# Kernel tuning notes

Hardware: AMD Instinct MI355X
Metric: run time of the kernel (lower is better)

## Reference

```python
import jax, jax.numpy as jnp
import numpy as np

B, T, D, H = 512, 256, 64, 256


def setup_inputs() -> dict:
    key = jax.random.key(0)
    ks = jax.random.split(key, 12)
    X = jax.random.normal(ks[0], (B, T, D), dtype=jnp.float32)
    M = (jax.random.uniform(ks[1], (B, T, D)) < 0.7).astype(jnp.float32)
    # time since last observation, hours
    Delta = jax.random.uniform(ks[2], (B, T, D), dtype=jnp.float32) * 5.0
    x_mean = jax.random.normal(ks[3], (D,), dtype=jnp.float32) * 0.1
    s = 1.0 / np.sqrt(D)
    sh = 1.0 / np.sqrt(H)
    # input-decay Linear(D->D), hidden-decay Linear(D->H)
    W_gx = jax.random.uniform(ks[4], (D, D), minval=-s, maxval=s, dtype=jnp.float32)
    b_gx = jnp.zeros((D,), jnp.float32)
    W_gh = jax.random.uniform(ks[5], (D, H), minval=-s, maxval=s, dtype=jnp.float32)
    b_gh = jnp.zeros((H,), jnp.float32)
    # stacked gate weights for [z, r, h_tilde]
    W_x = jax.random.uniform(ks[6], (3, D, H), minval=-s, maxval=s, dtype=jnp.float32)
    W_h = jax.random.uniform(ks[7], (3, H, H), minval=-sh, maxval=sh, dtype=jnp.float32)
    W_m = jax.random.uniform(ks[8], (3, D, H), minval=-s, maxval=s, dtype=jnp.float32)
    b_g = jnp.zeros((3, H), jnp.float32)
    W_cls = jax.random.uniform(ks[9], (H, 1), minval=-sh, maxval=sh, dtype=jnp.float32)
    b_cls = jnp.zeros((1,), jnp.float32)
    return dict(X=X, M=M, Delta=Delta, x_mean=x_mean,
                W_gx=W_gx, b_gx=b_gx, W_gh=W_gh, b_gh=b_gh,
                W_x=W_x, W_h=W_h, W_m=W_m, b_g=b_g,
                W_cls=W_cls, b_cls=b_cls)


def reference(X, M, Delta, x_mean, W_gx, b_gx, W_gh, b_gh,
              W_x, W_h, W_m, b_g, W_cls, b_cls):
    Bn, Tn, Dn = X.shape
    Hn = W_h.shape[-1]

    def step(carry, inp):
        h, x_prev = carry          # [B,H], [B,D]
        x, m, d = inp              # each [B,D]
        gamma_x = jnp.exp(-jax.nn.relu(d @ W_gx + b_gx))   # [B,D]
        gamma_h = jnp.exp(-jax.nn.relu(d @ W_gh + b_gh))   # [B,H]
        # mean imputation with input decay
        x_hat = m * x + (1.0 - m) * (gamma_x * x_prev + (1.0 - gamma_x) * x_mean)
        hd = gamma_h * h                                   # hidden decay
        z = jax.nn.sigmoid(x_hat @ W_x[0] + hd @ W_h[0] + m @ W_m[0] + b_g[0])
        r = jax.nn.sigmoid(x_hat @ W_x[1] + hd @ W_h[1] + m @ W_m[1] + b_g[1])
        h_tilde = jnp.tanh(x_hat @ W_x[2] + (r * hd) @ W_h[2] + m @ W_m[2] + b_g[2])
        h_new = (1.0 - z) * hd + z * h_tilde
        x_prev_new = m * x + (1.0 - m) * x_prev            # carry last observation
        return (h_new, x_prev_new), None

    h0 = jnp.zeros((Bn, Hn), X.dtype)
    xp0 = jnp.zeros((Bn, Dn), X.dtype)
    xs = (jnp.swapaxes(X, 0, 1), jnp.swapaxes(M, 0, 1), jnp.swapaxes(Delta, 0, 1))
    (h, _), _ = jax.lax.scan(step, (h0, xp0), xs)
    return (h @ W_cls + b_cls)[:, 0]   # [B], classifier(h).squeeze(-1)
```

## Files before the change

kernel.cpp:

```cpp
#include <hip/hip_runtime.h>


constexpr int Bn = 512, Tn = 256, Dn = 64, Hn = 256;
constexpr int BB = 16, NBLK = Bn / BB;
constexpr int TC = 128;

typedef __attribute__((ext_vector_type(8))) short bf8_t;
typedef __attribute__((ext_vector_type(4))) float f4_t;

constexpr size_t OFF_WH  = 0;
constexpr size_t OFF_WX  = 196608;
constexpr size_t OFF_WM  = 245760;
constexpr size_t OFF_WGH = 294912;
constexpr size_t OFF_WGX = 311296;
constexpr int    PACK_SLOTS = 39424;

constexpr size_t GX_OFF  = (size_t)1 << 20;
constexpr size_t GH_OFF  = GX_OFF + (size_t)Bn * Tn * Dn * 4;
constexpr size_t WS_NEED = GH_OFF + (size_t)Bn * Tn * Hn * 2;

constexpr size_t GH2_OFF = (size_t)1 << 20;
constexpr size_t GX2_OFF = GH2_OFF + (size_t)Bn * Tn * Hn * 2;
constexpr size_t P2_OFF  = GX2_OFF;
constexpr size_t P2_SZ   = (size_t)3 * Bn * TC * Hn * 2;
constexpr size_t XH2_OFF = P2_OFF + P2_SZ;
constexpr size_t HST_OFF = XH2_OFF + (size_t)Bn * Tn * Dn * 2;
constexpr size_t WS_NEED3 = HST_OFF + (size_t)Bn * Hn * 2;

__device__ __forceinline__ unsigned short f2bf(float x) {
    union { float f; unsigned int u; } v; v.f = x;
    unsigned int r = (v.u + 0x7fffu + ((v.u >> 16) & 1u)) >> 16;
    return (unsigned short)r;
}
__device__ __forceinline__ float bf2f(unsigned short u) {
    union { unsigned int i; float f; } v; v.i = ((unsigned int)u) << 16; return v.f;
}
__device__ __forceinline__ bf8_t LD8(const short* p) { return *(const bf8_t*)p; }
__device__ __forceinline__ f4_t MF(bf8_t a, bf8_t b, f4_t c) {
    return __builtin_amdgcn_mfma_f32_16x16x32_bf16(a, b, c, 0, 0, 0);
}
__device__ __forceinline__ f4_t MFp(bf8_t a, const short* bp, f4_t c) {
    return MF(a, LD8(bp), c);
}
__device__ __forceinline__ const short* BA(const short* p, int ntG, int KT, int kt, int lane) {
    return p + (((size_t)ntG * KT + kt) * 64 + lane) * 8;
}
__device__ __forceinline__ void lds_sync() {
    __builtin_amdgcn_sched_barrier(0);
    asm volatile("s_waitcnt lgkmcnt(0)" ::: "memory");
    __builtin_amdgcn_s_barrier();
    __builtin_amdgcn_sched_barrier(0);
}

__global__ __launch_bounds__(256) void pack_weights(
    const float* __restrict__ W_gx, const float* __restrict__ W_gh,
    const float* __restrict__ W_x,  const float* __restrict__ W_h,
    const float* __restrict__ W_m,  short* __restrict__ out)
{
    const int slot = blockIdx.x * 256 + threadIdx.x;
    if (slot >= PACK_SLOTS) return;

    const float* w; int ldn, l, kt, j, kbase;
    if (slot < 24576) {
        int g = slot >> 13, rem = slot & 8191;
        int ntG = rem >> 9, r2 = rem & 511;
        kt = r2 >> 6; l = r2 & 63;
        j = ntG * 16 + (l & 15);
        w = W_h + (size_t)g * Hn * Hn; ldn = Hn;
    } else if (slot < 30720) {
        int s = slot - 24576;
        int g = s >> 11, rem = s & 2047;
        int ntG = rem >> 7, r2 = rem & 127;
        kt = r2 >> 6; l = r2 & 63;
        j = ntG * 16 + (l & 15);
        w = W_x + (size_t)g * Dn * Hn; ldn = Hn;
    } else if (slot < 36864) {
        int s = slot - 30720;
        int g = s >> 11, rem = s & 2047;
        int ntG = rem >> 7, r2 = rem & 127;
        kt = r2 >> 6; l = r2 & 63;
        j = ntG * 16 + (l & 15);
        w = W_m + (size_t)g * Dn * Hn; ldn = Hn;
    } else if (slot < 38912) {
        int s = slot - 36864;
        int ntG = s >> 7, r2 = s & 127;
        kt = r2 >> 6; l = r2 & 63;
        j = ntG * 16 + (l & 15);
        w = W_gh; ldn = Hn;
    } else {
        int s = slot - 38912;
        int ntG = s >> 7, r2 = s & 127;
        kt = r2 >> 6; l = r2 & 63;
        j = ntG * 16 + (l & 15);
        w = W_gx; ldn = Dn;
    }
    kbase = kt * 32 + ((l >> 4) << 3);
    bf8_t v;
    #pragma unroll
    for (int i = 0; i < 8; ++i)
        v[i] = (short)f2bf(w[(size_t)(kbase + i) * ldn + j]);
    *(bf8_t*)&out[(size_t)slot * 8] = v;
}

__global__ __launch_bounds__(256) void grud_prepass(
    const float* __restrict__ Dl, const float* __restrict__ b_gx,
    const float* __restrict__ b_gh, const short* __restrict__ pk,
    float* __restrict__ gx, unsigned short* __restrict__ gh)
{
    __shared__ short sDf[2 * 64 * 8];
    const int tid = threadIdx.x, w = tid >> 6, lane = tid & 63;
    const int bt = blockIdx.x >> 8, t = blockIdx.x & 255;
    const int b0 = bt * 16;
    const int c15 = lane & 15, rowb = (lane >> 4) * 4;

    if (w < 2) {
        const int row = lane & 15, cb = w * 32 + ((lane >> 4) << 3);
        const float* p = Dl + ((size_t)(b0 + row) * Tn + t) * Dn + cb;
        float4 a = *(const float4*)p, b = *(const float4*)(p + 4);
        bf8_t v;
        v[0]=(short)f2bf(a.x); v[1]=(short)f2bf(a.y); v[2]=(short)f2bf(a.z); v[3]=(short)f2bf(a.w);
        v[4]=(short)f2bf(b.x); v[5]=(short)f2bf(b.y); v[6]=(short)f2bf(b.z); v[7]=(short)f2bf(b.w);
        *(bf8_t*)&sDf[(w * 64 + lane) * 8] = v;
    }
    __syncthreads();
    bf8_t df0 = *(const bf8_t*)&sDf[lane * 8];
    bf8_t df1 = *(const bf8_t*)&sDf[(64 + lane) * 8];

    #pragma unroll
    for (int i = 0; i < 4; ++i) {
        const int ntG = 4 * w + i;
        f4_t acc = {0.f, 0.f, 0.f, 0.f};
        acc = MFp(df0, BA(pk + OFF_WGH, ntG, 2, 0, lane), acc);
        acc = MFp(df1, BA(pk + OFF_WGH, ntG, 2, 1, lane), acc);
        const int col = ntG * 16 + c15;
        const float bb = b_gh[col];
        #pragma unroll
        for (int q = 0; q < 4; ++q) {
            const int r = rowb + q;
            gh[((size_t)(b0 + r) * Tn + t) * Hn + col] =
                f2bf(__expf(-fmaxf(acc[q] + bb, 0.f)));
        }
    }
    {
        f4_t acc = {0.f, 0.f, 0.f, 0.f};
        acc = MFp(df0, BA(pk + OFF_WGX, w, 2, 0, lane), acc);
        acc = MFp(df1, BA(pk + OFF_WGX, w, 2, 1, lane), acc);
        const int col = w * 16 + c15;
        const float bb = b_gx[col];
        #pragma unroll
        for (int q = 0; q < 4; ++q) {
            const int r = rowb + q;
            gx[((size_t)(b0 + r) * Tn + t) * Dn + col] =
                __expf(-fmaxf(acc[q] + bb, 0.f));
        }
    }
}

__global__ __launch_bounds__(256) void grud_xhat(
    const float* __restrict__ X, const float* __restrict__ M,
    const float* __restrict__ x_mean, const float* __restrict__ gx,
    unsigned short* __restrict__ XH)
{
    const int g = blockIdx.x * 256 + threadIdx.x;
    const int b = g >> 6, d = g & 63;
    const float xm = x_mean[d];
    float xp = 0.f;
    const size_t base = (size_t)b * Tn * Dn + d;
    for (int t = 0; t < Tn; ++t) {
        const size_t idx = base + (size_t)t * Dn;
        const float x = X[idx], m = M[idx], gv = gx[idx];
        const float xh = m * x + (1.f - m) * (gv * xp + (1.f - gv) * xm);
        xp = m * x + (1.f - m) * xp;
        XH[idx] = f2bf(xh);
    }
}

__global__ __launch_bounds__(256) void grud_pgemm_c(
    const float* __restrict__ M, const unsigned short* __restrict__ XH,
    const float* __restrict__ b_g, const short* __restrict__ pk,
    unsigned short* __restrict__ P, int t0)
{
    const int tid = threadIdx.x, w = tid >> 6, lane = tid & 63;
    const int c15 = lane & 15;
    const int bblk = blockIdx.x >> 7;
    const int tl = blockIdx.x & (TC - 1);
    const int b0 = bblk * 16, t = t0 + tl;

    const size_t abase = ((size_t)(b0 + (lane & 15)) * Tn + t) * Dn + ((lane >> 4) << 3);
    bf8_t xf[2], mf[2];
    #pragma unroll
    for (int kt = 0; kt < 2; ++kt) {
        uint4 xa = *(const uint4*)&XH[abase + kt * 32];
        union { uint4 u; bf8_t b; } cvt; cvt.u = xa;
        xf[kt] = cvt.b;
        float4 a = *(const float4*)&M[abase + kt * 32];
        float4 b = *(const float4*)&M[abase + kt * 32 + 4];
        bf8_t v;
        v[0]=(short)f2bf(a.x); v[1]=(short)f2bf(a.y); v[2]=(short)f2bf(a.z); v[3]=(short)f2bf(a.w);
        v[4]=(short)f2bf(b.x); v[5]=(short)f2bf(b.y); v[6]=(short)f2bf(b.z); v[7]=(short)f2bf(b.w);
        mf[kt] = v;
    }

    const size_t btl = (size_t)blockIdx.x;
    #pragma unroll
    for (int i = 0; i < 12; ++i) {
        const int p = w * 12 + i;
        const int gg = p >> 4, ntG = p & 15;
        f4_t acc = {0.f, 0.f, 0.f, 0.f};
        acc = MFp(xf[0], BA(pk + OFF_WX + (size_t)gg * 16384, ntG, 2, 0, lane), acc);
        acc = MFp(xf[1], BA(pk + OFF_WX + (size_t)gg * 16384, ntG, 2, 1, lane), acc);
        acc = MFp(mf[0], BA(pk + OFF_WM + (size_t)gg * 16384, ntG, 2, 0, lane), acc);
        acc = MFp(mf[1], BA(pk + OFF_WM + (size_t)gg * 16384, ntG, 2, 1, lane), acc);
        const float bb = b_g[gg * Hn + ntG * 16 + c15];
        ushort4 o;
        o.x = f2bf(acc[0] + bb); o.y = f2bf(acc[1] + bb);
        o.z = f2bf(acc[2] + bb); o.w = f2bf(acc[3] + bb);
        *(ushort4*)&P[((btl * 3 + gg) * 16 + ntG) * 256 + lane * 4] = o;
    }
}

__global__ __launch_bounds__(512, 2) void grud_rec16(
    const float* __restrict__ W_cls, const float* __restrict__ b_cls,
    const short* __restrict__ pk, const unsigned short* __restrict__ gh,
    const unsigned short* __restrict__ P, unsigned short* __restrict__ hst,
    float* __restrict__ out, int t0, int lastc)
{
    __shared__ short sWh1[16 * 8 * 64 * 8];
    __shared__ unsigned short sh_hb[16][264];
    __shared__ short sA_rhd[8 * 64 * 8];

    const int tid = threadIdx.x, w = tid >> 6, lane = tid & 63;
    const int c15 = lane & 15, rowb = (lane >> 4) * 4;
    const int b0 = blockIdx.x * BB;
    unsigned short* hs = hst + (size_t)blockIdx.x * 16 * Hn;

    bf8_t whz[2][8], whh[2][8];
    #pragma unroll
    for (int nt = 0; nt < 2; ++nt)
        #pragma unroll
        for (int kt = 0; kt < 8; ++kt) {
            whz[nt][kt] = LD8(BA(pk + OFF_WH,             2 * w + nt, 8, kt, lane));
            whh[nt][kt] = LD8(BA(pk + OFF_WH + 2 * 65536, 2 * w + nt, 8, kt, lane));
        }
    for (int c = tid; c < 8192; c += 512)
        *(uint4*)&sWh1[c * 8] = *(const uint4*)&pk[OFF_WH + 65536 + (size_t)c * 8];

    if (t0 == 0) {
        for (int i = tid; i < 16 * 264; i += 512) (&sh_hb[0][0])[i] = 0;
    } else {
        for (int i = tid; i < 16 * 256; i += 512) {
            const int r = i >> 8, c = i & 255;
            float hv = bf2f(hs[i]);
            float gv = bf2f(gh[((size_t)(b0 + r) * Tn + t0) * Hn + c]);
            sh_hb[r][c] = f2bf(gv * hv);
        }
    }

    unsigned short ghcd[2][4];
    {
        const int t1 = (t0 + 1 < Tn) ? (t0 + 1) : (Tn - 1);
        #pragma unroll
        for (int nt = 0; nt < 2; ++nt)
            #pragma unroll
            for (int q = 0; q < 4; ++q)
                ghcd[nt][q] = gh[((size_t)(b0 + rowb + q) * Tn + t1) * Hn + w * 32 + nt * 16 + c15];
    }
    ushort4 pz[2], pr[2], ph[2];
    {
        const size_t pbl = (size_t)blockIdx.x * TC;
        #pragma unroll
        for (int nt = 0; nt < 2; ++nt) {
            pz[nt] = *(const ushort4*)&P[((pbl * 3 + 0) * 16 + 2 * w + nt) * 256 + lane * 4];
            pr[nt] = *(const ushort4*)&P[((pbl * 3 + 1) * 16 + 2 * w + nt) * 256 + lane * 4];
            ph[nt] = *(const ushort4*)&P[((pbl * 3 + 2) * 16 + 2 * w + nt) * 256 + lane * 4];
        }
    }
    float hd_cd[2][4], zz[2][4];
    const f4_t z4 = {0.f, 0.f, 0.f, 0.f};
    __syncthreads();

    for (int tl = 0; tl < TC; ++tl) {
        const int last = (tl == TC - 1);
        const int tnl  = last ? (TC - 1) : (tl + 1);
        const int tg2  = (t0 + tl + 2 < Tn) ? (t0 + tl + 2) : (Tn - 1);

        unsigned short ghcd_n[2][4];
        #pragma unroll
        for (int nt = 0; nt < 2; ++nt)
            #pragma unroll
            for (int q = 0; q < 4; ++q)
                ghcd_n[nt][q] = gh[((size_t)(b0 + rowb + q) * Tn + tg2) * Hn + w * 32 + nt * 16 + c15];
        ushort4 pz_n[2], pr_n[2], ph_n[2];
        {
            const size_t pbl = (size_t)blockIdx.x * TC + tnl;
            #pragma unroll
            for (int nt = 0; nt < 2; ++nt) {
                pz_n[nt] = *(const ushort4*)&P[((pbl * 3 + 0) * 16 + 2 * w + nt) * 256 + lane * 4];
                pr_n[nt] = *(const ushort4*)&P[((pbl * 3 + 1) * 16 + 2 * w + nt) * 256 + lane * 4];
                ph_n[nt] = *(const ushort4*)&P[((pbl * 3 + 2) * 16 + 2 * w + nt) * 256 + lane * 4];
            }
        }
        #pragma unroll
        for (int nt = 0; nt < 2; ++nt)
            #pragma unroll
            for (int q = 0; q < 4; ++q)
                hd_cd[nt][q] = bf2f(sh_hb[rowb + q][w * 32 + nt * 16 + c15]);

        f4_t aZ[2] = {z4, z4}, aR[2] = {z4, z4};
        #pragma unroll
        for (int kt = 0; kt < 8; ++kt) {
            union { uint4 u; bf8_t b; } hf;
            hf.u = *(const uint4*)&sh_hb[lane & 15][kt * 32 + ((lane >> 4) << 3)];
            bf8_t wr0 = LD8(&sWh1[((2 * w + 0) * 8 + kt) * 512 + lane * 8]);
            bf8_t wr1 = LD8(&sWh1[((2 * w + 1) * 8 + kt) * 512 + lane * 8]);
            aZ[0] = MF(hf.b, whz[0][kt], aZ[0]);
            aZ[1] = MF(hf.b, whz[1][kt], aZ[1]);
            aR[0] = MF(hf.b, wr0, aR[0]);
            aR[1] = MF(hf.b, wr1, aR[1]);
        }
        #pragma unroll
        for (int nt = 0; nt < 2; ++nt) {
            const int col = w * 32 + nt * 16 + c15;
            #pragma unroll
            for (int q = 0; q < 4; ++q) {
                const int r = rowb + q;
                float z  = 1.f / (1.f + __expf(-(aZ[nt][q] + bf2f(((const unsigned short*)&pz[nt])[q]))));
                float rr = 1.f / (1.f + __expf(-(aR[nt][q] + bf2f(((const unsigned short*)&pr[nt])[q]))));
                zz[nt][q] = z;
                sA_rhd[(w * 64 + ((col & 31) >> 3) * 16 + r) * 8 + (col & 7)] =
                    (short)f2bf(rr * hd_cd[nt][q]);
            }
        }
        lds_sync();

        f4_t aH[2] = {z4, z4};
        #pragma unroll
        for (int kt = 0; kt < 8; ++kt) {
            bf8_t rf = LD8(&sA_rhd[(kt * 64 + lane) * 8]);
            aH[0] = MF(rf, whh[0][kt], aH[0]);
            aH[1] = MF(rf, whh[1][kt], aH[1]);
        }
        #pragma unroll
        for (int nt = 0; nt < 2; ++nt) {
            const int col = w * 32 + nt * 16 + c15;
            #pragma unroll
            for (int q = 0; q < 4; ++q) {
                const int r = rowb + q;
                float pre = aH[nt][q] + bf2f(((const unsigned short*)&ph[nt])[q]);
                float a = fabsf(pre), e = __expf(-2.f * a);
                float th = copysignf((1.f - e) / (1.f + e), pre);
                float hn = (1.f - zz[nt][q]) * hd_cd[nt][q] + zz[nt][q] * th;
                float sv = last ? hn : hn * bf2f(ghcd[nt][q]);
                sh_hb[r][col] = f2bf(sv);
            }
        }
        lds_sync();

        #pragma unroll
        for (int nt = 0; nt < 2; ++nt) {
            #pragma unroll
            for (int q = 0; q < 4; ++q) ghcd[nt][q] = ghcd_n[nt][q];
            pz[nt] = pz_n[nt]; pr[nt] = pr_n[nt]; ph[nt] = ph_n[nt];
        }
    }

    if (!lastc) {
        for (int i = tid; i < 16 * 256; i += 512)
            hs[i] = sh_hb[i >> 8][i & 255];
    } else {
        #pragma unroll
        for (int rr2 = 0; rr2 < 2; ++rr2) {
            const int row = w * 2 + rr2;
            ushort4 hb = *(const ushort4*)&sh_hb[row][lane * 4];
            float4 wv  = *(const float4*)&W_cls[lane * 4];
            float p = bf2f(hb.x) * wv.x + bf2f(hb.y) * wv.y +
                      bf2f(hb.z) * wv.z + bf2f(hb.w) * wv.w;
            #pragma unroll
            for (int o = 32; o > 0; o >>= 1) p += __shfl_down(p, o, 64);
            if (lane == 0) out[b0 + row] = p + b_cls[0];
        }
    }
}

__global__ __launch_bounds__(512, 2) void grud_rec8(
    const float* __restrict__ X, const float* __restrict__ M,
    const float* __restrict__ x_mean, const float* __restrict__ b_g,
    const float* __restrict__ W_cls, const float* __restrict__ b_cls,
    const short* __restrict__ pk, const float* __restrict__ gx,
    const unsigned short* __restrict__ gh, float* __restrict__ out)
{
    __shared__ short sWh1[16 * 8 * 64 * 8];
    __shared__ unsigned short sh_hb[16][264];
    __shared__ short sA_xh[2 * 64 * 8];
    __shared__ short sA_m [2 * 64 * 8];
    __shared__ short sA_hd[8 * 64 * 8];
    __shared__ short sA_rhd[8 * 64 * 8];

    const int tid = threadIdx.x, w = tid >> 6, lane = tid & 63;
    const int c15 = lane & 15, rowb = (lane >> 4) * 4;
    const int b0 = blockIdx.x * BB;

    bf8_t whz[2][8], whh[2][8];
    #pragma unroll
    for (int nt = 0; nt < 2; ++nt)
        #pragma unroll
        for (int kt = 0; kt < 8; ++kt) {
            whz[nt][kt] = LD8(BA(pk + OFF_WH,             2 * w + nt, 8, kt, lane));
            whh[nt][kt] = LD8(BA(pk + OFF_WH + 2 * 65536, 2 * w + nt, 8, kt, lane));
        }
    for (int c = tid; c < 8192; c += 512)
        *(uint4*)&sWh1[c * 8] = *(const uint4*)&pk[OFF_WH + 65536 + (size_t)c * 8];
    for (int i = tid; i < 16 * 264; i += 512) (&sh_hb[0][0])[i] = 0;

    const float bz[2] = { b_g[0 * Hn + w * 32 + c15], b_g[0 * Hn + w * 32 + 16 + c15] };
    const float brr[2]= { b_g[1 * Hn + w * 32 + c15], b_g[1 * Hn + w * 32 + 16 + c15] };
    const float bh[2] = { b_g[2 * Hn + w * 32 + c15], b_g[2 * Hn + w * 32 + 16 + c15] };

    const int s    = w * 32 + (lane & 31);
    const int kt2  = s >> 7, fl = (s >> 1) & 63, half = s & 1;
    const int brow = fl & 15, bcol = kt2 * 32 + ((fl >> 4) << 3) + half * 4;
    const size_t brow_base = ((size_t)(b0 + brow) * Tn) * Dn + bcol;

    float xb[4] = {0.f, 0.f, 0.f, 0.f};
    float xp[4] = {0.f, 0.f, 0.f, 0.f};
    float4 mv, xv = {0,0,0,0}, gxv = {0,0,0,0};
    if (lane < 32) {
        xb[0]=x_mean[bcol]; xb[1]=x_mean[bcol+1]; xb[2]=x_mean[bcol+2]; xb[3]=x_mean[bcol+3];
        xv  = *(const float4*)&X[brow_base];
        gxv = *(const float4*)&gx[brow_base];
    }
    mv = *(const float4*)&M[brow_base];

    const size_t ghA_base  = ((size_t)(b0 + (lane & 15)) * Tn) * Hn + w * 32 + ((lane >> 4) << 3);
    uint4 gha = *(const uint4*)&gh[ghA_base];
    unsigned short ghcd[2][4];
    #pragma unroll
    for (int nt = 0; nt < 2; ++nt)
        #pragma unroll
        for (int q = 0; q < 4; ++q)
            ghcd[nt][q] = gh[((size_t)(b0 + rowb + q) * Tn) * Hn + w * 32 + nt * 16 + c15];

    float h_cd[2][4] = {{0.f,0.f,0.f,0.f},{0.f,0.f,0.f,0.f}};
    float hd_cd[2][4], zz[2][4];
    const f4_t z4 = {0.f, 0.f, 0.f, 0.f};
    __syncthreads();

    for (int t = 0; t < Tn; ++t) {
        const int tn = (t + 1 < Tn) ? (t + 1) : (Tn - 1);

        {
            uint4 hA = *(const uint4*)&sh_hb[lane & 15][w * 32 + ((lane >> 4) << 3)];
            unsigned int ga[4] = {gha.x, gha.y, gha.z, gha.w};
            unsigned int ha[4] = {hA.x, hA.y, hA.z, hA.w};
            bf8_t hv;
            #pragma unroll
            for (int i = 0; i < 8; ++i) {
                float gf = bf2f((unsigned short)((ga[i >> 1] >> ((i & 1) * 16)) & 0xffffu));
                float hf = bf2f((unsigned short)((ha[i >> 1] >> ((i & 1) * 16)) & 0xffffu));
                hv[i] = (short)f2bf(gf * hf);
            }
            *(bf8_t*)&sA_hd[(w * 64 + lane) * 8] = hv;
        }
        #pragma unroll
        for (int nt = 0; nt < 2; ++nt)
            #pragma unroll
            for (int q = 0; q < 4; ++q)
                hd_cd[nt][q] = bf2f(ghcd[nt][q]) * h_cd[nt][q];

        if (lane < 32) {
            float mm[4] = {mv.x, mv.y, mv.z, mv.w};
            float xx[4] = {xv.x, xv.y, xv.z, xv.w};
            float gg[4] = {gxv.x, gxv.y, gxv.z, gxv.w};
            float xh[4];
            #pragma unroll
            for (int j = 0; j < 4; ++j) {
                xh[j] = mm[j] * xx[j] + (1.f - mm[j]) * (gg[j] * xp[j] + (1.f - gg[j]) * xb[j]);
                xp[j] = mm[j] * xx[j] + (1.f - mm[j]) * xp[j];
            }
            uint2 dd;
            dd.x = (unsigned int)f2bf(xh[0]) | ((unsigned int)f2bf(xh[1]) << 16);
            dd.y = (unsigned int)f2bf(xh[2]) | ((unsigned int)f2bf(xh[3]) << 16);
            *(uint2*)&sA_xh[(kt2 * 64 + fl) * 8 + half * 4] = dd;
        } else {
            uint2 dd;
            dd.x = (unsigned int)f2bf(mv.x) | ((unsigned int)f2bf(mv.y) << 16);
            dd.y = (unsigned int)f2bf(mv.z) | ((unsigned int)f2bf(mv.w) << 16);
            *(uint2*)&sA_m[(kt2 * 64 + fl) * 8 + half * 4] = dd;
        }
        {
            const size_t ba = brow_base + (size_t)tn * Dn;
            mv = *(const float4*)&M[ba];
            if (lane < 32) {
                xv  = *(const float4*)&X[ba];
                gxv = *(const float4*)&gx[ba];
            }
            gha = *(const uint4*)&gh[ghA_base + (size_t)tn * Hn];
            #pragma unroll
            for (int nt = 0; nt < 2; ++nt)
                #pragma unroll
                for (int q = 0; q < 4; ++q)
                    ghcd[nt][q] = gh[((size_t)(b0 + rowb + q) * Tn + tn) * Hn + w * 32 + nt * 16 + c15];
        }
        lds_sync();

        bf8_t wxz[2][2], wxr[2][2], wmz[2][2], wmr[2][2];
        #pragma unroll
        for (int nt = 0; nt < 2; ++nt)
            #pragma unroll
            for (int kt = 0; kt < 2; ++kt) {
                wxz[nt][kt] = LD8(BA(pk + OFF_WX,         2 * w + nt, 2, kt, lane));
                wxr[nt][kt] = LD8(BA(pk + OFF_WX + 16384, 2 * w + nt, 2, kt, lane));
                wmz[nt][kt] = LD8(BA(pk + OFF_WM,         2 * w + nt, 2, kt, lane));
                wmr[nt][kt] = LD8(BA(pk + OFF_WM + 16384, 2 * w + nt, 2, kt, lane));
            }
        bf8_t xf0 = LD8(&sA_xh[lane * 8]), xf1 = LD8(&sA_xh[(64 + lane) * 8]);
        bf8_t mf0 = LD8(&sA_m [lane * 8]), mf1 = LD8(&sA_m [(64 + lane) * 8]);

        f4_t aZ[2] = {z4, z4}, aR[2] = {z4, z4};
        #pragma unroll
        for (int kt = 0; kt < 8; ++kt) {
            bf8_t hf  = LD8(&sA_hd[(kt * 64 + lane) * 8]);
            bf8_t wr0 = LD8(&sWh1[((2 * w + 0) * 8 + kt) * 512 + lane * 8]);
            bf8_t wr1 = LD8(&sWh1[((2 * w + 1) * 8 + kt) * 512 + lane * 8]);
            aZ[0] = MF(hf, whz[0][kt], aZ[0]);
            aZ[1] = MF(hf, whz[1][kt], aZ[1]);
            aR[0] = MF(hf, wr0, aR[0]);
            aR[1] = MF(hf, wr1, aR[1]);
        }
        #pragma unroll
        for (int nt = 0; nt < 2; ++nt) {
            aZ[nt] = MF(xf0, wxz[nt][0], aZ[nt]); aZ[nt] = MF(xf1, wxz[nt][1], aZ[nt]);
            aZ[nt] = MF(mf0, wmz[nt][0], aZ[nt]); aZ[nt] = MF(mf1, wmz[nt][1], aZ[nt]);
            aR[nt] = MF(xf0, wxr[nt][0], aR[nt]); aR[nt] = MF(xf1, wxr[nt][1], aR[nt]);
            aR[nt] = MF(mf0, wmr[nt][0], aR[nt]); aR[nt] = MF(mf1, wmr[nt][1], aR[nt]);
        }
        bf8_t wxh[2][2], wmh[2][2];
        #pragma unroll
        for (int nt = 0; nt < 2; ++nt)
            #pragma unroll
            for (int kt = 0; kt < 2; ++kt) {
                wxh[nt][kt] = LD8(BA(pk + OFF_WX + 32768, 2 * w + nt, 2, kt, lane));
                wmh[nt][kt] = LD8(BA(pk + OFF_WM + 32768, 2 * w + nt, 2, kt, lane));
            }
        #pragma unroll
        for (int nt = 0; nt < 2; ++nt) {
            const int col = w * 32 + nt * 16 + c15;
            #pragma unroll
            for (int q = 0; q < 4; ++q) {
                const int r = rowb + q;
                float z  = 1.f / (1.f + __expf(-(aZ[nt][q] + bz[nt])));
                float rr = 1.f / (1.f + __expf(-(aR[nt][q] + brr[nt])));
                zz[nt][q] = z;
                sA_rhd[(w * 64 + ((col & 31) >> 3) * 16 + r) * 8 + (col & 7)] =
                    (short)f2bf(rr * hd_cd[nt][q]);
            }
        }
        lds_sync();

        f4_t aH[2] = {z4, z4};
        #pragma unroll
        for (int kt = 0; kt < 8; ++kt) {
            bf8_t rf = LD8(&sA_rhd[(kt * 64 + lane) * 8]);
            aH[0] = MF(rf, whh[0][kt], aH[0]);
            aH[1] = MF(rf, whh[1][kt], aH[1]);
        }
        #pragma unroll
        for (int nt = 0; nt < 2; ++nt) {
            aH[nt] = MF(xf0, wxh[nt][0], aH[nt]); aH[nt] = MF(xf1, wxh[nt][1], aH[nt]);
            aH[nt] = MF(mf0, wmh[nt][0], aH[nt]); aH[nt] = MF(mf1, wmh[nt][1], aH[nt]);
        }
        #pragma unroll
        for (int nt = 0; nt < 2; ++nt) {
            const int col = w * 32 + nt * 16 + c15;
            #pragma unroll
            for (int q = 0; q < 4; ++q) {
                const int r = rowb + q;
                float pre = aH[nt][q] + bh[nt];
                float a = fabsf(pre), e = __expf(-2.f * a);
                float th = copysignf((1.f - e) / (1.f + e), pre);
                float hn = (1.f - zz[nt][q]) * hd_cd[nt][q] + zz[nt][q] * th;
                h_cd[nt][q] = hn;
                sh_hb[r][col] = f2bf(hn);
            }
        }
        lds_sync();
    }

    #pragma unroll
    for (int rr2 = 0; rr2 < 2; ++rr2) {
        const int row = w * 2 + rr2;
        ushort4 hb = *(const ushort4*)&sh_hb[row][lane * 4];
        float4 wv  = *(const float4*)&W_cls[lane * 4];
        float p = bf2f(hb.x) * wv.x + bf2f(hb.y) * wv.y +
                  bf2f(hb.z) * wv.z + bf2f(hb.w) * wv.w;
        #pragma unroll
        for (int o = 32; o > 0; o >>= 1) p += __shfl_down(p, o, 64);
        if (lane == 0) out[b0 + row] = p + b_cls[0];
    }
}

extern "C" void kernel_launch(void* const* d_in, const int* in_sizes, int n_in,
                              void* d_out, int out_size, void* d_ws, size_t ws_size,
                              hipStream_t stream) {
    const float* X      = (const float*)d_in[0];
    const float* M      = (const float*)d_in[1];
    const float* Dl     = (const float*)d_in[2];
    const float* x_mean = (const float*)d_in[3];
    const float* W_gx   = (const float*)d_in[4];
    const float* b_gx   = (const float*)d_in[5];
    const float* W_gh   = (const float*)d_in[6];
    const float* b_gh   = (const float*)d_in[7];
    const float* W_x    = (const float*)d_in[8];
    const float* W_h    = (const float*)d_in[9];
    const float* W_m    = (const float*)d_in[10];
    const float* b_g    = (const float*)d_in[11];
    const float* W_cls  = (const float*)d_in[12];
    const float* b_cls  = (const float*)d_in[13];
    float* out = (float*)d_out;
    short* pk  = (short*)d_ws;

    hipLaunchKernelGGL(pack_weights, dim3((PACK_SLOTS + 255) / 256), dim3(256), 0, stream,
                       W_gx, W_gh, W_x, W_h, W_m, pk);

    if (ws_size >= WS_NEED3) {
        unsigned short* gh2 = (unsigned short*)((char*)d_ws + GH2_OFF);
        float*          gx2 = (float*)((char*)d_ws + GX2_OFF);
        unsigned short* P2  = (unsigned short*)((char*)d_ws + P2_OFF);
        unsigned short* xh2 = (unsigned short*)((char*)d_ws + XH2_OFF);
        unsigned short* hst = (unsigned short*)((char*)d_ws + HST_OFF);

        hipLaunchKernelGGL(grud_prepass, dim3(NBLK * Tn), dim3(256), 0, stream,
                           Dl, b_gx, b_gh, pk, gx2, gh2);
        hipLaunchKernelGGL(grud_xhat, dim3(Bn * Dn / 256), dim3(256), 0, stream,
                           X, M, x_mean, gx2, xh2);
        for (int c = 0; c < Tn / TC; ++c) {
            hipLaunchKernelGGL(grud_pgemm_c, dim3(NBLK * TC), dim3(256), 0, stream,
                               M, xh2, b_g, pk, P2, c * TC);
            hipLaunchKernelGGL(grud_rec16, dim3(NBLK), dim3(512), 0, stream,
                               W_cls, b_cls, pk, gh2, P2, hst, out,
                               c * TC, (c == Tn / TC - 1) ? 1 : 0);
        }
    } else {
        float*          gxbuf = (float*)((char*)d_ws + GX_OFF);
        unsigned short* ghbuf = (unsigned short*)((char*)d_ws + GH_OFF);
        hipLaunchKernelGGL(grud_prepass, dim3(NBLK * Tn), dim3(256), 0, stream,
                           Dl, b_gx, b_gh, pk, gxbuf, ghbuf);
        hipLaunchKernelGGL(grud_rec8, dim3(NBLK), dim3(512), 0, stream,
                           X, M, x_mean, b_g, W_cls, b_cls, pk, gxbuf, ghbuf, out);
    }
}
```

Before: 977.8 us.

## Overlap next-chunk input projection GEMM with recurrence using extra producer blocks

Adds extra blocks to the recurrence kernel launch that compute the input-projection GEMM for the next time chunk into a second buffer while the 32 recurrence blocks process the current chunk. This double-buffers P and removes one standalone pgemm launch from the serial path, filling otherwise idle CUs during the latency-bound recurrence. It risks contention for memory bandwidth and L2 with the recurrence blocks, and it needs a larger workspace, falling back to the old path if the workspace is too small.

```diff
diff --git a/kernel.cpp b/kernel.cpp
--- a/kernel.cpp
+++ b/kernel.cpp
@@ -4,6 +4,7 @@
 constexpr int Bn = 512, Tn = 256, Dn = 64, Hn = 256;
 constexpr int BB = 16, NBLK = Bn / BB;
 constexpr int TC = 128;
+constexpr int PGB = 128;
 
 typedef __attribute__((ext_vector_type(8))) short bf8_t;
 typedef __attribute__((ext_vector_type(4))) float f4_t;
@@ -26,6 +27,12 @@
 constexpr size_t XH2_OFF = P2_OFF + P2_SZ;
 constexpr size_t HST_OFF = XH2_OFF + (size_t)Bn * Tn * Dn * 2;
 constexpr size_t WS_NEED3 = HST_OFF + (size_t)Bn * Hn * 2;
+
+constexpr size_t P4A_OFF = GX2_OFF;
+constexpr size_t P4B_OFF = P4A_OFF + P2_SZ;
+constexpr size_t XH4_OFF = P4B_OFF + P2_SZ;
+constexpr size_t HST4_OFF = XH4_OFF + (size_t)Bn * Tn * Dn * 2;
+constexpr size_t WS_NEED4 = HST4_OFF + (size_t)Bn * Hn * 2;
 
 __device__ __forceinline__ unsigned short f2bf(float x) {
     union { float f; unsigned int u; } v; v.f = x;
@@ -175,15 +182,14 @@
     }
 }
 
-__global__ __launch_bounds__(256) void grud_pgemm_c(
+__device__ __forceinline__ void pgemm_tile(
     const float* __restrict__ M, const unsigned short* __restrict__ XH,
     const float* __restrict__ b_g, const short* __restrict__ pk,
-    unsigned short* __restrict__ P, int t0)
+    unsigned short* __restrict__ P, int tile, int t0, int w, int lane)
 {
-    const int tid = threadIdx.x, w = tid >> 6, lane = tid & 63;
     const int c15 = lane & 15;
-    const int bblk = blockIdx.x >> 7;
-    const int tl = blockIdx.x & (TC - 1);
+    const int bblk = tile >> 7;
+    const int tl = tile & (TC - 1);
     const int b0 = bblk * 16, t = t0 + tl;
 
     const size_t abase = ((size_t)(b0 + (lane & 15)) * Tn + t) * Dn + ((lane >> 4) << 3);
@@ -200,8 +206,7 @@
         v[4]=(short)f2bf(b.x); v[5]=(short)f2bf(b.y); v[6]=(short)f2bf(b.z); v[7]=(short)f2bf(b.w);
         mf[kt] = v;
     }
-
-    const size_t btl = (size_t)blockIdx.x;
+    const size_t btl = (size_t)tile;
     #pragma unroll
     for (int i = 0; i < 12; ++i) {
         const int p = w * 12 + i;
@@ -219,17 +224,41 @@
     }
 }
 
-__global__ __launch_bounds__(512, 2) void grud_rec16(
+__global__ __launch_bounds__(256) void grud_pgemm_c(
+    const float* __restrict__ M, const unsigned short* __restrict__ XH,
+    const float* __restrict__ b_g, const short* __restrict__ pk,
+    unsigned short* __restrict__ P, int t0)
+{
+    pgemm_tile(M, XH, b_g, pk, P, blockIdx.x, t0,
+               threadIdx.x >> 6, threadIdx.x & 63);
+}
+
+__global__ __launch_bounds__(512, 2) void grud_rec17(
     const float* __restrict__ W_cls, const float* __restrict__ b_cls,
     const short* __restrict__ pk, const unsigned short* __restrict__ gh,
-    const unsigned short* __restrict__ P, unsigned short* __restrict__ hst,
-    float* __restrict__ out, int t0, int lastc)
+    const unsigned short* __restrict__ P, unsigned short* __restrict__ Pn,
+    unsigned short* __restrict__ hst, float* __restrict__ out,
+    int t0, int lastc, int pgen,
+    const float* __restrict__ M, const unsigned short* __restrict__ XH,
+    const float* __restrict__ b_g)
 {
     __shared__ short sWh1[16 * 8 * 64 * 8];
     __shared__ unsigned short sh_hb[16][264];
     __shared__ short sA_rhd[8 * 64 * 8];
 
     const int tid = threadIdx.x, w = tid >> 6, lane = tid & 63;
+
+    if (blockIdx.x >= NBLK) {
+        if (!pgen) return;
+        const int pb = blockIdx.x - NBLK;
+        const int half = tid >> 8, htid = tid & 255;
+        const int wp = htid >> 6, lanep = htid & 63;
+        const int t0n = t0 + TC;
+        for (int u = pb * 2 + half; u < NBLK * TC; u += PGB * 2)
+            pgemm_tile(M, XH, b_g, pk, Pn, u, t0n, wp, lanep);
+        return;
+    }
+
     const int c15 = lane & 15, rowb = (lane >> 4) * 4;
     const int b0 = blockIdx.x * BB;
     unsigned short* hs = hst + (size_t)blockIdx.x * 16 * Hn;
@@ -622,7 +651,27 @@
     hipLaunchKernelGGL(pack_weights, dim3((PACK_SLOTS + 255) / 256), dim3(256), 0, stream,
                        W_gx, W_gh, W_x, W_h, W_m, pk);
 
-    if (ws_size >= WS_NEED3) {
+    if (ws_size >= WS_NEED4) {
+        unsigned short* gh2 = (unsigned short*)((char*)d_ws + GH2_OFF);
+        float*          gx2 = (float*)((char*)d_ws + GX2_OFF);
+        unsigned short* PA  = (unsigned short*)((char*)d_ws + P4A_OFF);
+        unsigned short* PB  = (unsigned short*)((char*)d_ws + P4B_OFF);
+        unsigned short* xh2 = (unsigned short*)((char*)d_ws + XH4_OFF);
+        unsigned short* hst = (unsigned short*)((char*)d_ws + HST4_OFF);
+
+        hipLaunchKernelGGL(grud_prepass, dim3(NBLK * Tn), dim3(256), 0, stream,
+                           Dl, b_gx, b_gh, pk, gx2, gh2);
+        hipLaunchKernelGGL(grud_xhat, dim3(Bn * Dn / 256), dim3(256), 0, stream,
+                           X, M, x_mean, gx2, xh2);
+        hipLaunchKernelGGL(grud_pgemm_c, dim3(NBLK * TC), dim3(256), 0, stream,
+                           M, xh2, b_g, pk, PA, 0);
+        hipLaunchKernelGGL(grud_rec17, dim3(NBLK + PGB), dim3(512), 0, stream,
+                           W_cls, b_cls, pk, gh2, PA, PB, hst, out,
+                           0, 0, 1, M, xh2, b_g);
+        hipLaunchKernelGGL(grud_rec17, dim3(NBLK), dim3(512), 0, stream,
+                           W_cls, b_cls, pk, gh2, PB, PA, hst, out,
+                           TC, 1, 0, M, xh2, b_g);
+    } else if (ws_size >= WS_NEED3) {
         unsigned short* gh2 = (unsigned short*)((char*)d_ws + GH2_OFF);
         float*          gx2 = (float*)((char*)d_ws + GX2_OFF);
         unsigned short* P2  = (unsigned short*)((char*)d_ws + P2_OFF);
@@ -636,9 +685,9 @@
         for (int c = 0; c < Tn / TC; ++c) {
             hipLaunchKernelGGL(grud_pgemm_c, dim3(NBLK * TC), dim3(256), 0, stream,
                                M, xh2, b_g, pk, P2, c * TC);
-            hipLaunchKernelGGL(grud_rec16, dim3(NBLK), dim3(512), 0, stream,
-                               W_cls, b_cls, pk, gh2, P2, hst, out,
-                               c * TC, (c == Tn / TC - 1) ? 1 : 0);
+            hipLaunchKernelGGL(grud_rec17, dim3(NBLK), dim3(512), 0, stream,
+                               W_cls, b_cls, pk, gh2, P2, P2, hst, out,
+                               c * TC, (c == Tn / TC - 1) ? 1 : 0, 0, M, xh2, b_g);
         }
     } else {
         float*          gxbuf = (float*)((char*)d_ws + GX_OFF);
```

Measured after the change: 985.5 us. Within noise of the previous version (+0.8%).
